# Performance work log

Measured on AMD Instinct MI355X. Metric: run time of the kernel, lower is better.

The kernel has to match this reference:

```python
import jax, jax.numpy as jnp
import numpy as np

N_NODES = 50000
N_EDGES = 800000
NF = 128
HC = 128
NC = 40


def sage_conv(x, src, dst, Wl, Wr, b, num_nodes):
    """PyG SAGEConv with mean aggregation:
    out = lin_l(mean_{j in N(i)} x_j) + lin_r(x_i), bias folded into lin_l."""
    msgs = x[src]                                             # [E, F] gather
    agg = jax.ops.segment_sum(msgs, dst, num_segments=num_nodes)  # [N, F]
    cnt = jax.ops.segment_sum(jnp.ones((src.shape[0],), dtype=x.dtype), dst,
                              num_segments=num_nodes)          # [N]
    mean = agg / jnp.clip(cnt, 1.0)[:, None]                   # mean aggregation
    return mean @ Wl.T + x @ Wr.T + b


def setup_inputs() -> dict:
    key = jax.random.key(0)
    k = jax.random.split(key, 8)
    x = jax.random.normal(k[0], (N_NODES, NF), dtype=jnp.float32)
    edge_index = jax.random.randint(k[1], (2, N_EDGES), 0, N_NODES, dtype=jnp.int32)
    s1 = 1.0 / np.sqrt(NF)
    s2 = 1.0 / np.sqrt(HC)
    Wl1 = jax.random.uniform(k[2], (HC, NF), jnp.float32, -s1, s1)
    Wr1 = jax.random.uniform(k[3], (HC, NF), jnp.float32, -s1, s1)
    b1 = jnp.zeros((HC,), jnp.float32)
    Wl2 = jax.random.uniform(k[4], (NC, HC), jnp.float32, -s2, s2)
    Wr2 = jax.random.uniform(k[5], (NC, HC), jnp.float32, -s2, s2)
    b2 = jnp.zeros((NC,), jnp.float32)
    return {"x": x, "edge_index": edge_index, "Wl1": Wl1, "Wr1": Wr1,
            "b1": b1, "Wl2": Wl2, "Wr2": Wr2, "b2": b2}


def reference(x, edge_index, Wl1, Wr1, b1, Wl2, Wr2, b2):
    src, dst = edge_index[0], edge_index[1]
    num_nodes = x.shape[0]
    emb = sage_conv(x, src, dst, Wl1, Wr1, b1, num_nodes)      # embedding_output
    h = jax.nn.relu(emb)
    # F.dropout with training=False is the identity (inference reference)
    logits = sage_conv(h, src, dst, Wl2, Wr2, b2, num_nodes)
    return (logits, emb)
```

## Files before the change

### kernel.cpp

```cpp
#include <hip/hip_runtime.h>
#include <hip/hip_bf16.h>
#include <stdint.h>

#define NODES 50000
#define EDGES 800000
#define CAP   64

typedef __attribute__((ext_vector_type(8))) short bf16x8;
typedef __attribute__((ext_vector_type(8))) unsigned short u16x8;
typedef __attribute__((ext_vector_type(4))) float f32x4;
typedef unsigned short ushort_t;

__device__ __forceinline__ float4 ld4(const float* p) {
    return *reinterpret_cast<const float4*>(p);
}
__device__ __forceinline__ ushort_t f2bf(float f) {
    unsigned u = __float_as_uint(f);
    unsigned r = (u + 0x7fff + ((u >> 16) & 1)) >> 16;
    return (ushort_t)r;
}
__device__ __forceinline__ float bf2f(ushort_t h) {
    return __uint_as_float(((unsigned)h) << 16);
}

__global__ __launch_bounds__(256) void zerok(int* __restrict__ deg) {
    int t = blockIdx.x * 256 + threadIdx.x;
    if (t < 25000) reinterpret_cast<int2*>(deg)[t] = make_int2(0, 0);
}

__global__ __launch_bounds__(256) void prep(
    const float* __restrict__ x, const int* __restrict__ src,
    const int* __restrict__ dst,
    const float* __restrict__ Wr1, const float* __restrict__ Wl1,
    const float* __restrict__ Wr2, const float* __restrict__ Wl2,
    int* __restrict__ deg, ushort_t* __restrict__ esrc,
    ushort_t* __restrict__ xbf, ushort_t* __restrict__ w1p,
    ushort_t* __restrict__ w2p) {
    int b = blockIdx.x;
    if (b < 3128) {
        int g = b & 7, chunk = b >> 3;
        int lo = g * 6250;
#pragma unroll
        for (int k = 0; k < 8; ++k) {
            int e = chunk * 2048 + k * 256 + threadIdx.x;
            if (e < EDGES) {
                int d = dst[e];
                if ((unsigned)(d - lo) < 6250u) {
                    int s = src[e];
                    int p = atomicAdd(&deg[d], 1);
                    if (p < CAP) esrc[(size_t)d * CAP + p] = (ushort_t)s;
                }
            }
        }
    } else if (b < 9378) {
        int idx = (b - 3128) * 256 + threadIdx.x;
        int i = idx >> 5, c = idx & 31;
        float4 v = ld4(x + (size_t)i * 128 + c * 4);
        ushort4 h;
        h.x = f2bf(v.x); h.y = f2bf(v.y); h.z = f2bf(v.z); h.w = f2bf(v.w);
        *reinterpret_cast<ushort4*>(xbf + (size_t)i * 128 + c * 4) = h;
    } else if (b < 9394) {
        int t = (b - 9378) * 256 + threadIdx.x;
        int nf = t >> 9, kc = (t >> 6) & 7, lane = t & 63;
        int r = nf * 16 + (lane & 15);
        int k2 = kc * 32 + ((lane >> 4) << 3);
        u16x8 o;
#pragma unroll
        for (int j = 0; j < 8; ++j) {
            int kk = k2 + j;
            float v = (kk < 128) ? Wr1[r * 128 + kk] : Wl1[r * 128 + (kk - 128)];
            o[j] = f2bf(v);
        }
        *reinterpret_cast<u16x8*>(w1p + (size_t)t * 8) = o;
    } else {
        int t = (b - 9394) * 256 + threadIdx.x;
        if (t >= 1280) return;
        int nf = t >> 8, kc = (t >> 6) & 3, lane = t & 63;
        int r = nf * 16 + (lane & 15);
        int k2 = kc * 32 + ((lane >> 4) << 3);
        u16x8 o;
#pragma unroll
        for (int j = 0; j < 8; ++j) {
            int kk = k2 + j;
            float v = (r < 40) ? Wr2[r * 128 + kk] : Wl2[(r - 40) * 128 + kk];
            o[j] = f2bf(v);
        }
        *reinterpret_cast<u16x8*>(w2p + (size_t)t * 8) = o;
    }
}

__global__ __launch_bounds__(256) void gemm12(
    const ushort_t* __restrict__ xbf, const ushort_t* __restrict__ esrc,
    const int* __restrict__ deg, const ushort_t* __restrict__ w1p,
    const ushort_t* __restrict__ w2p, const float* __restrict__ b1,
    float* __restrict__ emb, ushort_t* __restrict__ V, int M) {
    __shared__ ushort_t ms[64][136];
    __shared__ ushort_t hs[64][136];
    const int tid = threadIdx.x;
    const int row0 = blockIdx.x * 64;

    {
        const int c = tid & 15, rloc = tid >> 4;
#pragma unroll
        for (int p = 0; p < 4; ++p) {
            int rr = p * 16 + rloc;
            int i = row0 + rr;
            int dg = (i < M) ? deg[i] : 0;
            int n = dg < CAP ? dg : CAP;
            if (i >= M) n = 0;
            const ushort_t* ep = esrc + (size_t)i * CAP;
            float a0[8] = {}, a1[8] = {};
            int j = 0;
            for (; j + 8 <= n; j += 8) {
                int s0 = ep[j],     s1 = ep[j + 1], s2 = ep[j + 2], s3 = ep[j + 3];
                int s4 = ep[j + 4], s5 = ep[j + 5], s6 = ep[j + 6], s7 = ep[j + 7];
                u16x8 v0 = *reinterpret_cast<const u16x8*>(xbf + (size_t)s0 * 128 + c * 8);
                u16x8 v1 = *reinterpret_cast<const u16x8*>(xbf + (size_t)s1 * 128 + c * 8);
                u16x8 v2 = *reinterpret_cast<const u16x8*>(xbf + (size_t)s2 * 128 + c * 8);
                u16x8 v3 = *reinterpret_cast<const u16x8*>(xbf + (size_t)s3 * 128 + c * 8);
                u16x8 v4 = *reinterpret_cast<const u16x8*>(xbf + (size_t)s4 * 128 + c * 8);
                u16x8 v5 = *reinterpret_cast<const u16x8*>(xbf + (size_t)s5 * 128 + c * 8);
                u16x8 v6 = *reinterpret_cast<const u16x8*>(xbf + (size_t)s6 * 128 + c * 8);
                u16x8 v7 = *reinterpret_cast<const u16x8*>(xbf + (size_t)s7 * 128 + c * 8);
#pragma unroll
                for (int k = 0; k < 8; ++k) {
                    a0[k] += (bf2f(v0[k]) + bf2f(v2[k])) + (bf2f(v4[k]) + bf2f(v6[k]));
                    a1[k] += (bf2f(v1[k]) + bf2f(v3[k])) + (bf2f(v5[k]) + bf2f(v7[k]));
                }
            }
            for (; j + 4 <= n; j += 4) {
                int s0 = ep[j], s1 = ep[j + 1], s2 = ep[j + 2], s3 = ep[j + 3];
                u16x8 v0 = *reinterpret_cast<const u16x8*>(xbf + (size_t)s0 * 128 + c * 8);
                u16x8 v1 = *reinterpret_cast<const u16x8*>(xbf + (size_t)s1 * 128 + c * 8);
                u16x8 v2 = *reinterpret_cast<const u16x8*>(xbf + (size_t)s2 * 128 + c * 8);
                u16x8 v3 = *reinterpret_cast<const u16x8*>(xbf + (size_t)s3 * 128 + c * 8);
#pragma unroll
                for (int k = 0; k < 8; ++k) {
                    a0[k] += bf2f(v0[k]) + bf2f(v2[k]);
                    a1[k] += bf2f(v1[k]) + bf2f(v3[k]);
                }
            }
            for (; j < n; ++j) {
                int s = ep[j];
                u16x8 v = *reinterpret_cast<const u16x8*>(xbf + (size_t)s * 128 + c * 8);
#pragma unroll
                for (int k = 0; k < 8; ++k) a0[k] += bf2f(v[k]);
            }
            float ci = 1.0f / fmaxf((float)dg, 1.0f);
            u16x8 m;
#pragma unroll
            for (int k = 0; k < 8; ++k) m[k] = f2bf((a0[k] + a1[k]) * ci);
            *reinterpret_cast<u16x8*>(&ms[rr][c * 8]) = m;
        }
    }
    __syncthreads();

    const int wave = tid >> 6, lane = tid & 63;
    int arow = row0 + wave * 16 + (lane & 15); if (arow >= M) arow = M - 1;
    const int rtile = wave * 16 + (lane & 15);
    const int klane = (lane >> 4) * 8;

    f32x4 acc[8] = {};
#pragma unroll
    for (int kc = 0; kc < 8; ++kc) {
        bf16x8 a = (kc < 4)
            ? *reinterpret_cast<const bf16x8*>(xbf + (size_t)arow * 128 + kc * 32 + klane)
            : *reinterpret_cast<const bf16x8*>(&ms[rtile][(kc - 4) * 32 + klane]);
        bf16x8 wv[8];
#pragma unroll
        for (int nf = 0; nf < 8; ++nf)
            wv[nf] = *reinterpret_cast<const bf16x8*>(
                w1p + (size_t)((nf * 8 + kc) * 64 + lane) * 8);
#pragma unroll
        for (int nf = 0; nf < 8; ++nf)
            acc[nf] = __builtin_amdgcn_mfma_f32_16x16x32_bf16(a, wv[nf], acc[nf], 0, 0, 0);
    }

    const int crow0r = wave * 16 + (lane >> 4) * 4;
    const int crow0  = row0 + crow0r;
    const int ccol   = lane & 15;
#pragma unroll
    for (int nf = 0; nf < 8; ++nf) {
        int col = nf * 16 + ccol;
        float bv = b1[col];
#pragma unroll
        for (int r = 0; r < 4; ++r) {
            int row = crow0 + r;
            float val = acc[nf][r] + bv;
            if (row < M)
                __builtin_nontemporal_store(val, emb + (size_t)row * 128 + col);
            hs[crow0r + r][col] = f2bf(fmaxf(val, 0.f));
        }
    }
    __syncthreads();

    f32x4 acc2[5] = {};
#pragma unroll
    for (int kc = 0; kc < 4; ++kc) {
        bf16x8 a = *reinterpret_cast<const bf16x8*>(&hs[rtile][kc * 32 + klane]);
        bf16x8 wv[5];
#pragma unroll
        for (int nf = 0; nf < 5; ++nf)
            wv[nf] = *reinterpret_cast<const bf16x8*>(
                w2p + (size_t)((nf * 4 + kc) * 64 + lane) * 8);
#pragma unroll
        for (int nf = 0; nf < 5; ++nf)
            acc2[nf] = __builtin_amdgcn_mfma_f32_16x16x32_bf16(a, wv[nf], acc2[nf], 0, 0, 0);
    }
#pragma unroll
    for (int nf = 0; nf < 5; ++nf) {
        int col = nf * 16 + ccol;
#pragma unroll
        for (int r = 0; r < 4; ++r) {
            int row = crow0 + r;
            if (row < M) V[(size_t)row * 80 + col] = f2bf(acc2[nf][r]);
        }
    }
}

__global__ __launch_bounds__(256) void agg2(
    const ushort_t* __restrict__ V, const ushort_t* __restrict__ esrc,
    const int* __restrict__ deg, const float* __restrict__ b2,
    float* __restrict__ logits) {
    int idx = blockIdx.x * 256 + threadIdx.x;
    int i = idx >> 3, c = idx & 7;
    if (i >= NODES || c >= 5) return;
    int dg = deg[i];
    int n = dg < CAP ? dg : CAP;
    const ushort_t* ep = esrc + (size_t)i * CAP;
    float a0[8] = {}, a1[8] = {};
    int j = 0;
    for (; j + 8 <= n; j += 8) {
        int s0 = ep[j],     s1 = ep[j + 1], s2 = ep[j + 2], s3 = ep[j + 3];
        int s4 = ep[j + 4], s5 = ep[j + 5], s6 = ep[j + 6], s7 = ep[j + 7];
        u16x8 v0 = *reinterpret_cast<const u16x8*>(V + (size_t)s0 * 80 + 40 + c * 8);
        u16x8 v1 = *reinterpret_cast<const u16x8*>(V + (size_t)s1 * 80 + 40 + c * 8);
        u16x8 v2 = *reinterpret_cast<const u16x8*>(V + (size_t)s2 * 80 + 40 + c * 8);
        u16x8 v3 = *reinterpret_cast<const u16x8*>(V + (size_t)s3 * 80 + 40 + c * 8);
        u16x8 v4 = *reinterpret_cast<const u16x8*>(V + (size_t)s4 * 80 + 40 + c * 8);
        u16x8 v5 = *reinterpret_cast<const u16x8*>(V + (size_t)s5 * 80 + 40 + c * 8);
        u16x8 v6 = *reinterpret_cast<const u16x8*>(V + (size_t)s6 * 80 + 40 + c * 8);
        u16x8 v7 = *reinterpret_cast<const u16x8*>(V + (size_t)s7 * 80 + 40 + c * 8);
#pragma unroll
        for (int k = 0; k < 8; ++k) {
            a0[k] += (bf2f(v0[k]) + bf2f(v2[k])) + (bf2f(v4[k]) + bf2f(v6[k]));
            a1[k] += (bf2f(v1[k]) + bf2f(v3[k])) + (bf2f(v5[k]) + bf2f(v7[k]));
        }
    }
    for (; j + 4 <= n; j += 4) {
        int s0 = ep[j], s1 = ep[j + 1], s2 = ep[j + 2], s3 = ep[j + 3];
        u16x8 v0 = *reinterpret_cast<const u16x8*>(V + (size_t)s0 * 80 + 40 + c * 8);
        u16x8 v1 = *reinterpret_cast<const u16x8*>(V + (size_t)s1 * 80 + 40 + c * 8);
        u16x8 v2 = *reinterpret_cast<const u16x8*>(V + (size_t)s2 * 80 + 40 + c * 8);
        u16x8 v3 = *reinterpret_cast<const u16x8*>(V + (size_t)s3 * 80 + 40 + c * 8);
#pragma unroll
        for (int k = 0; k < 8; ++k) {
            a0[k] += bf2f(v0[k]) + bf2f(v2[k]);
            a1[k] += bf2f(v1[k]) + bf2f(v3[k]);
        }
    }
    for (; j < n; ++j) {
        int s = ep[j];
        u16x8 v = *reinterpret_cast<const u16x8*>(V + (size_t)s * 80 + 40 + c * 8);
#pragma unroll
        for (int k = 0; k < 8; ++k) a0[k] += bf2f(v[k]);
    }
    float ci = 1.0f / fmaxf((float)dg, 1.0f);
    u16x8 sv = *reinterpret_cast<const u16x8*>(V + (size_t)i * 80 + c * 8);
    float o[8];
#pragma unroll
    for (int k = 0; k < 8; ++k)
        o[k] = bf2f(sv[k]) + (a0[k] + a1[k]) * ci + b2[c * 8 + k];
    float4* dst4 = reinterpret_cast<float4*>(logits + (size_t)i * 40 + c * 8);
    dst4[0] = make_float4(o[0], o[1], o[2], o[3]);
    dst4[1] = make_float4(o[4], o[5], o[6], o[7]);
}

extern "C" void kernel_launch(void* const* d_in, const int* in_sizes, int n_in,
                              void* d_out, int out_size, void* d_ws, size_t ws_size,
                              hipStream_t stream) {
    const float* x   = (const float*)d_in[0];
    const int*   ei  = (const int*)d_in[1];
    const float* Wl1 = (const float*)d_in[2];
    const float* Wr1 = (const float*)d_in[3];
    const float* b1  = (const float*)d_in[4];
    const float* Wl2 = (const float*)d_in[5];
    const float* Wr2 = (const float*)d_in[6];
    const float* b2  = (const float*)d_in[7];
    const int* src = ei;
    const int* dst = ei + EDGES;

    char* ws = (char*)d_ws;
    ushort_t* xbf  = (ushort_t*)ws;
    ushort_t* V    = (ushort_t*)(ws + 12800000);
    ushort_t* esrc = (ushort_t*)(ws + 20800000);
    int*      deg  = (int*)(ws + 27200000);
    ushort_t* w1p  = (ushort_t*)(ws + 27400000);
    ushort_t* w2p  = (ushort_t*)(ws + 27465536);

    float* logits_out = (float*)d_out;
    float* emb_out    = logits_out + (size_t)NODES * 40;

    zerok<<<98, 256, 0, stream>>>(deg);

    prep<<<9399, 256, 0, stream>>>(x, src, dst, Wr1, Wl1, Wr2, Wl2,
                                   deg, esrc, xbf, w1p, w2p);

    gemm12<<<(NODES + 63) / 64, 256, 0, stream>>>(xbf, esrc, deg, w1p, w2p, b1,
                                                  emb_out, V, NODES);

    agg2<<<(NODES * 8 + 255) / 256, 256, 0, stream>>>(V, esrc, deg, b2, logits_out);
}
```

Baseline: 130.1 us.

## Split neighbor mean aggregation out of fused GEMM kernel into separate pass

Moves the layer-1 neighbor gather and mean from the shared-memory prologue of gemm12 into a standalone aggx kernel that writes a bf16 mean buffer to global memory. gemm12 then reads the mean rows directly from global memory instead of a shared-memory tile. The aim is to run the latency-bound gather at full occupancy without the GEMM's register and LDS pressure, and to drop one barrier and 17 KB of LDS from gemm12. The cost is an extra kernel launch and a 12.8 MB write plus read of the intermediate.

Result: faster. 120.0 us (-7.8%).

```diff
diff --git a/kernel.cpp b/kernel.cpp
--- a/kernel.cpp
+++ b/kernel.cpp
@@ -89,75 +89,67 @@
     }
 }
 
+__global__ __launch_bounds__(256) void aggx(
+    const ushort_t* __restrict__ xbf, ushort_t* __restrict__ mbf,
+    const ushort_t* __restrict__ esrc, const int* __restrict__ deg) {
+    int idx = blockIdx.x * 256 + threadIdx.x;
+    int i = idx >> 4, c = idx & 15;
+    int dg = deg[i];
+    int n = dg < CAP ? dg : CAP;
+    const ushort_t* ep = esrc + (size_t)i * CAP;
+    float a0[8] = {}, a1[8] = {};
+    int j = 0;
+    for (; j + 8 <= n; j += 8) {
+        int s0 = ep[j],     s1 = ep[j + 1], s2 = ep[j + 2], s3 = ep[j + 3];
+        int s4 = ep[j + 4], s5 = ep[j + 5], s6 = ep[j + 6], s7 = ep[j + 7];
+        u16x8 v0 = *reinterpret_cast<const u16x8*>(xbf + (size_t)s0 * 128 + c * 8);
+        u16x8 v1 = *reinterpret_cast<const u16x8*>(xbf + (size_t)s1 * 128 + c * 8);
+        u16x8 v2 = *reinterpret_cast<const u16x8*>(xbf + (size_t)s2 * 128 + c * 8);
+        u16x8 v3 = *reinterpret_cast<const u16x8*>(xbf + (size_t)s3 * 128 + c * 8);
+        u16x8 v4 = *reinterpret_cast<const u16x8*>(xbf + (size_t)s4 * 128 + c * 8);
+        u16x8 v5 = *reinterpret_cast<const u16x8*>(xbf + (size_t)s5 * 128 + c * 8);
+        u16x8 v6 = *reinterpret_cast<const u16x8*>(xbf + (size_t)s6 * 128 + c * 8);
+        u16x8 v7 = *reinterpret_cast<const u16x8*>(xbf + (size_t)s7 * 128 + c * 8);
+#pragma unroll
+        for (int k = 0; k < 8; ++k) {
+            a0[k] += (bf2f(v0[k]) + bf2f(v2[k])) + (bf2f(v4[k]) + bf2f(v6[k]));
+            a1[k] += (bf2f(v1[k]) + bf2f(v3[k])) + (bf2f(v5[k]) + bf2f(v7[k]));
+        }
+    }
+    for (; j + 4 <= n; j += 4) {
+        int s0 = ep[j], s1 = ep[j + 1], s2 = ep[j + 2], s3 = ep[j + 3];
+        u16x8 v0 = *reinterpret_cast<const u16x8*>(xbf + (size_t)s0 * 128 + c * 8);
+        u16x8 v1 = *reinterpret_cast<const u16x8*>(xbf + (size_t)s1 * 128 + c * 8);
+        u16x8 v2 = *reinterpret_cast<const u16x8*>(xbf + (size_t)s2 * 128 + c * 8);
+        u16x8 v3 = *reinterpret_cast<const u16x8*>(xbf + (size_t)s3 * 128 + c * 8);
+#pragma unroll
+        for (int k = 0; k < 8; ++k) {
+            a0[k] += bf2f(v0[k]) + bf2f(v2[k]);
+            a1[k] += bf2f(v1[k]) + bf2f(v3[k]);
+        }
+    }
+    for (; j < n; ++j) {
+        int s = ep[j];
+        u16x8 v = *reinterpret_cast<const u16x8*>(xbf + (size_t)s * 128 + c * 8);
+#pragma unroll
+        for (int k = 0; k < 8; ++k) a0[k] += bf2f(v[k]);
+    }
+    float ci = 1.0f / fmaxf((float)dg, 1.0f);
+    u16x8 m;
+#pragma unroll
+    for (int k = 0; k < 8; ++k) m[k] = f2bf((a0[k] + a1[k]) * ci);
+    *reinterpret_cast<u16x8*>(mbf + (size_t)i * 128 + c * 8) = m;
+}
+
 __global__ __launch_bounds__(256) void gemm12(
-    const ushort_t* __restrict__ xbf, const ushort_t* __restrict__ esrc,
-    const int* __restrict__ deg, const ushort_t* __restrict__ w1p,
-    const ushort_t* __restrict__ w2p, const float* __restrict__ b1,
-    float* __restrict__ emb, ushort_t* __restrict__ V, int M) {
-    __shared__ ushort_t ms[64][136];
+    const ushort_t* __restrict__ xbf, const ushort_t* __restrict__ mbf,
+    const ushort_t* __restrict__ w1p, const ushort_t* __restrict__ w2p,
+    const float* __restrict__ b1, float* __restrict__ emb,
+    ushort_t* __restrict__ V, int M) {
     __shared__ ushort_t hs[64][136];
-    const int tid = threadIdx.x;
-    const int row0 = blockIdx.x * 64;
-
-    {
-        const int c = tid & 15, rloc = tid >> 4;
-#pragma unroll
-        for (int p = 0; p < 4; ++p) {
-            int rr = p * 16 + rloc;
-            int i = row0 + rr;
-            int dg = (i < M) ? deg[i] : 0;
-            int n = dg < CAP ? dg : CAP;
-            if (i >= M) n = 0;
-            const ushort_t* ep = esrc + (size_t)i * CAP;
-            float a0[8] = {}, a1[8] = {};
-            int j = 0;
-            for (; j + 8 <= n; j += 8) {
-                int s0 = ep[j],     s1 = ep[j + 1], s2 = ep[j + 2], s3 = ep[j + 3];
-                int s4 = ep[j + 4], s5 = ep[j + 5], s6 = ep[j + 6], s7 = ep[j + 7];
-                u16x8 v0 = *reinterpret_cast<const u16x8*>(xbf + (size_t)s0 * 128 + c * 8);
-                u16x8 v1 = *reinterpret_cast<const u16x8*>(xbf + (size_t)s1 * 128 + c * 8);
-                u16x8 v2 = *reinterpret_cast<const u16x8*>(xbf + (size_t)s2 * 128 + c * 8);
-                u16x8 v3 = *reinterpret_cast<const u16x8*>(xbf + (size_t)s3 * 128 + c * 8);
-                u16x8 v4 = *reinterpret_cast<const u16x8*>(xbf + (size_t)s4 * 128 + c * 8);
-                u16x8 v5 = *reinterpret_cast<const u16x8*>(xbf + (size_t)s5 * 128 + c * 8);
-                u16x8 v6 = *reinterpret_cast<const u16x8*>(xbf + (size_t)s6 * 128 + c * 8);
-                u16x8 v7 = *reinterpret_cast<const u16x8*>(xbf + (size_t)s7 * 128 + c * 8);
-#pragma unroll
-                for (int k = 0; k < 8; ++k) {
-                    a0[k] += (bf2f(v0[k]) + bf2f(v2[k])) + (bf2f(v4[k]) + bf2f(v6[k]));
-                    a1[k] += (bf2f(v1[k]) + bf2f(v3[k])) + (bf2f(v5[k]) + bf2f(v7[k]));
-                }
-            }
-            for (; j + 4 <= n; j += 4) {
-                int s0 = ep[j], s1 = ep[j + 1], s2 = ep[j + 2], s3 = ep[j + 3];
-                u16x8 v0 = *reinterpret_cast<const u16x8*>(xbf + (size_t)s0 * 128 + c * 8);
-                u16x8 v1 = *reinterpret_cast<const u16x8*>(xbf + (size_t)s1 * 128 + c * 8);
-                u16x8 v2 = *reinterpret_cast<const u16x8*>(xbf + (size_t)s2 * 128 + c * 8);
-                u16x8 v3 = *reinterpret_cast<const u16x8*>(xbf + (size_t)s3 * 128 + c * 8);
-#pragma unroll
-                for (int k = 0; k < 8; ++k) {
-                    a0[k] += bf2f(v0[k]) + bf2f(v2[k]);
-                    a1[k] += bf2f(v1[k]) + bf2f(v3[k]);
-                }
-            }
-            for (; j < n; ++j) {
-                int s = ep[j];
-                u16x8 v = *reinterpret_cast<const u16x8*>(xbf + (size_t)s * 128 + c * 8);
-#pragma unroll
-                for (int k = 0; k < 8; ++k) a0[k] += bf2f(v[k]);
-            }
-            float ci = 1.0f / fmaxf((float)dg, 1.0f);
-            u16x8 m;
-#pragma unroll
-            for (int k = 0; k < 8; ++k) m[k] = f2bf((a0[k] + a1[k]) * ci);
-            *reinterpret_cast<u16x8*>(&ms[rr][c * 8]) = m;
-        }
-    }
-    __syncthreads();
-
-    const int wave = tid >> 6, lane = tid & 63;
-    int arow = row0 + wave * 16 + (lane & 15); if (arow >= M) arow = M - 1;
-    const int rtile = wave * 16 + (lane & 15);
+    const int wave = threadIdx.x >> 6, lane = threadIdx.x & 63;
+    const int r0 = blockIdx.x * 64 + wave * 16;
+    int arow = r0 + (lane & 15); if (arow >= M) arow = M - 1;
     const int klane = (lane >> 4) * 8;
 
     f32x4 acc[8] = {};
@@ -165,7 +157,7 @@
     for (int kc = 0; kc < 8; ++kc) {
         bf16x8 a = (kc < 4)
             ? *reinterpret_cast<const bf16x8*>(xbf + (size_t)arow * 128 + kc * 32 + klane)
-            : *reinterpret_cast<const bf16x8*>(&ms[rtile][(kc - 4) * 32 + klane]);
+            : *reinterpret_cast<const bf16x8*>(mbf + (size_t)arow * 128 + (kc - 4) * 32 + klane);
         bf16x8 wv[8];
 #pragma unroll
         for (int nf = 0; nf < 8; ++nf)
@@ -177,7 +169,7 @@
     }
 
     const int crow0r = wave * 16 + (lane >> 4) * 4;
-    const int crow0  = row0 + crow0r;
+    const int crow0  = blockIdx.x * 64 + crow0r;
     const int ccol   = lane & 15;
 #pragma unroll
     for (int nf = 0; nf < 8; ++nf) {
@@ -197,7 +189,8 @@
     f32x4 acc2[5] = {};
 #pragma unroll
     for (int kc = 0; kc < 4; ++kc) {
-        bf16x8 a = *reinterpret_cast<const bf16x8*>(&hs[rtile][kc * 32 + klane]);
+        bf16x8 a = *reinterpret_cast<const bf16x8*>(
+            &hs[wave * 16 + (lane & 15)][kc * 32 + klane]);
         bf16x8 wv[5];
 #pragma unroll
         for (int nf = 0; nf < 5; ++nf)
@@ -292,11 +285,12 @@
 
     char* ws = (char*)d_ws;
     ushort_t* xbf  = (ushort_t*)ws;
-    ushort_t* V    = (ushort_t*)(ws + 12800000);
-    ushort_t* esrc = (ushort_t*)(ws + 20800000);
-    int*      deg  = (int*)(ws + 27200000);
-    ushort_t* w1p  = (ushort_t*)(ws + 27400000);
-    ushort_t* w2p  = (ushort_t*)(ws + 27465536);
+    ushort_t* mbf  = (ushort_t*)(ws + 12800000);
+    ushort_t* V    = (ushort_t*)(ws + 25600000);
+    ushort_t* esrc = (ushort_t*)(ws + 33600000);
+    int*      deg  = (int*)(ws + 40000000);
+    ushort_t* w1p  = (ushort_t*)(ws + 40200000);
+    ushort_t* w2p  = (ushort_t*)(ws + 40265536);
 
     float* logits_out = (float*)d_out;
     float* emb_out    = logits_out + (size_t)NODES * 40;
@@ -306,7 +300,9 @@
     prep<<<9399, 256, 0, stream>>>(x, src, dst, Wr1, Wl1, Wr2, Wl2,
                                    deg, esrc, xbf, w1p, w2p);
 
-    gemm12<<<(NODES + 63) / 64, 256, 0, stream>>>(xbf, esrc, deg, w1p, w2p, b1,
+    aggx<<<3125, 256, 0, stream>>>(xbf, mbf, esrc, deg);
+
+    gemm12<<<(NODES + 63) / 64, 256, 0, stream>>>(xbf, mbf, w1p, w2p, b1,
                                                   emb_out, V, NODES);
 
     agg2<<<(NODES * 8 + 255) / 256, 256, 0, stream>>>(V, esrc, deg, b2, logits_out);
```
